# Performance work log

Measured on AMD Instinct MI355X. Metric: run time of the kernel, lower is better.

The kernel has to match this reference:

```python
import jax, jax.numpy as jnp
import numpy as np

NUM_HEADS = 16
HEAD_DIM = 64  # hidden_size 1024 / 16 heads


def setup_inputs() -> dict:
    key = jax.random.key(0)
    ks = jax.random.split(key, 5)
    B, S, D = 4, 2048, 1024
    std = 0.02
    return {
        "hidden_states": jax.random.normal(ks[0], (B, S, D), jnp.float32),
        "attention_mask": jnp.zeros((B, 1, 1, S), jnp.float32),
        "Wq": jax.random.normal(ks[1], (D, D), jnp.float32) * std,
        "bq": jnp.zeros((D,), jnp.float32),
        "Wk": jax.random.normal(ks[2], (D, D), jnp.float32) * std,
        "bk": jnp.zeros((D,), jnp.float32),
        "Wv": jax.random.normal(ks[3], (D, D), jnp.float32) * std,
        "bv": jnp.zeros((D,), jnp.float32),
    }


def _split_heads(x):
    # [B, S, H*dh] -> [B, H, S, dh]
    B, S, _ = x.shape
    return x.reshape(B, S, NUM_HEADS, HEAD_DIM).transpose(0, 2, 1, 3)


def reference(hidden_states, attention_mask, Wq, bq, Wk, bk, Wv, bv):
    q = _split_heads(hidden_states @ Wq + bq)  # [B,H,S,dh]
    k = _split_heads(hidden_states @ Wk + bk)
    v = _split_heads(hidden_states @ Wv + bv)
    scale = 1.0 / jnp.sqrt(jnp.asarray(HEAD_DIM, q.dtype))
    scores = jnp.einsum("bhqd,bhkd->bhqk", q, k) * scale
    scores = scores + attention_mask.astype(scores.dtype)
    probs = jax.nn.softmax(scores, axis=-1)  # dropout prob = 0 -> identity
    ctx = jnp.einsum("bhqk,bhkd->bhqd", probs, v)
    B, H, S, dh = ctx.shape
    return ctx.transpose(0, 2, 1, 3).reshape(B, S, H * dh)
```

## Files before the change

### kernel.cpp

```cpp
#include <hip/hip_runtime.h>
#include <stdint.h>

typedef unsigned short u16;
typedef __attribute__((ext_vector_type(4))) float f32x4;
typedef __attribute__((ext_vector_type(8))) short bf16x8;
typedef __attribute__((ext_vector_type(4))) short bf16x4;
typedef __attribute__((ext_vector_type(4))) int i32x4;

__device__ inline u16 f2b(float x) {
  union { float f; uint32_t u; } t; t.f = x;
  uint32_t r = t.u + 0x7FFFu + ((t.u >> 16) & 1u);
  return (u16)(r >> 16);
}

__global__ void cvt_hs_k(const float* __restrict__ in, u16* __restrict__ outp, int n) {
  int i = (blockIdx.x * 256 + threadIdx.x) * 4;
  if (i >= n) return;
  float4 v = *(const float4*)(in + i);
  ushort4 o = { f2b(v.x), f2b(v.y), f2b(v.z), f2b(v.w) };
  *(ushort4*)(outp + i) = o;
}

__global__ void twk(const float* __restrict__ Wq, const float* __restrict__ Wk,
                    const float* __restrict__ Wv, u16* __restrict__ Wt) {
  __shared__ float tile[64][65];
  const float* W = (blockIdx.z == 0) ? Wq : ((blockIdx.z == 1) ? Wk : Wv);
  int n0 = blockIdx.x * 64, k0 = blockIdx.y * 64;
  int tid = threadIdx.x;
#pragma unroll 4
  for (int i = 0; i < 16; ++i) {
    int idx = i * 256 + tid; int r = idx >> 6, c = idx & 63;
    tile[r][c] = W[(k0 + r) * 1024 + n0 + c];
  }
  __syncthreads();
  u16* dst = Wt + blockIdx.z * 1048576;
#pragma unroll 4
  for (int i = 0; i < 16; ++i) {
    int idx = i * 256 + tid; int r = idx >> 6, c = idx & 63;
    dst[(n0 + r) * 1024 + k0 + c] = f2b(tile[c][r]);
  }
}

__global__ __launch_bounds__(256) void qkv_gemm_k(
    const u16* __restrict__ hsb, const u16* __restrict__ wt,
    const float* __restrict__ bq, const float* __restrict__ bk, const float* __restrict__ bv,
    u16* __restrict__ Qo, u16* __restrict__ Ko, u16* __restrict__ Vto) {
  __shared__ u16 t1[128 * 64];
  __shared__ u16 t2[128 * 64];
  const int tid = threadIdx.x;
  const int w = tid >> 6, l = tid & 63, g = l >> 4, lm = l & 15;
  const int nbase = blockIdx.x * 128;
  const int wi = nbase >> 10;
  const int nloc0 = nbase & 1023;
  const int mbase = blockIdx.y * 128;
  const bool swapped = (wi < 2);
  const u16* T1g = swapped ? (wt + wi * 1048576 + nloc0 * 1024) : (hsb + mbase * 1024);
  const u16* T2g = swapped ? (hsb + mbase * 1024) : (wt + 2 * 1048576 + nloc0 * 1024);

  f32x4 acc[4][4];
#pragma unroll
  for (int i = 0; i < 4; ++i)
#pragma unroll
    for (int j = 0; j < 4; ++j)
#pragma unroll
      for (int r = 0; r < 4; ++r) acc[i][j][r] = 0.f;

  const int r1w = (w >> 1) * 64;
  const int r2w = (w & 1) * 64;

  for (int kb = 0; kb < 1024; kb += 64) {
    __syncthreads();
#pragma unroll
    for (int p = 0; p < 4; ++p) {
      int idx = p * 256 + tid;
      int r = idx >> 3, c = idx & 7;
      int sc = ((c ^ (r & 7)) * 8);
      *(i32x4*)(t1 + r * 64 + sc) = *(const i32x4*)(T1g + r * 1024 + kb + c * 8);
      *(i32x4*)(t2 + r * 64 + sc) = *(const i32x4*)(T2g + r * 1024 + kb + c * 8);
    }
    __syncthreads();
#pragma unroll
    for (int ks = 0; ks < 2; ++ks) {
      bf16x8 fa[4], fb[4];
#pragma unroll
      for (int i = 0; i < 4; ++i) {
        int ra = r1w + i * 16 + lm;
        fa[i] = *(const bf16x8*)(t1 + ra * 64 + (((g + 4 * ks) ^ (ra & 7)) * 8));
        int rb = r2w + i * 16 + lm;
        fb[i] = *(const bf16x8*)(t2 + rb * 64 + (((g + 4 * ks) ^ (rb & 7)) * 8));
      }
#pragma unroll
      for (int i = 0; i < 4; ++i)
#pragma unroll
        for (int j = 0; j < 4; ++j)
          acc[i][j] = __builtin_amdgcn_mfma_f32_16x16x32_bf16(fa[i], fb[j], acc[i][j], 0, 0, 0);
    }
  }

  if (swapped) {
    u16* O = (wi == 0) ? Qo : Ko;
    const float* bias = (wi == 0) ? bq : bk;
#pragma unroll
    for (int i = 0; i < 4; ++i) {
      int nl = nloc0 + r1w + i * 16 + g * 4;
      f32x4 bv4 = *(const f32x4*)(bias + nl);
      int d = nl & 63, h = nl >> 6;
#pragma unroll
      for (int j = 0; j < 4; ++j) {
        int m = mbase + r2w + j * 16 + lm;
        int bb = m >> 11, s = m & 2047;
        f32x4 v = acc[i][j];
        ushort4 o = { f2b(v[0] + bv4[0]), f2b(v[1] + bv4[1]),
                      f2b(v[2] + bv4[2]), f2b(v[3] + bv4[3]) };
        *(ushort4*)(O + ((size_t)(bb * 16 + h) * 2048 + s) * 64 + d) = o;
      }
    }
  } else {
#pragma unroll
    for (int j = 0; j < 4; ++j) {
      int nl = nloc0 + r2w + j * 16 + lm;
      float bias = bv[nl];
      int d = nl & 63, h = nl >> 6;
#pragma unroll
      for (int i = 0; i < 4; ++i) {
        int m = mbase + r1w + i * 16 + g * 4;
        int bb = m >> 11, s = m & 2047;
        f32x4 v = acc[i][j];
        ushort4 o = { f2b(v[0] + bias), f2b(v[1] + bias),
                      f2b(v[2] + bias), f2b(v[3] + bias) };
        *(ushort4*)(Vto + ((size_t)(bb * 16 + h) * 64 + d) * 2048 + s) = o;
      }
    }
  }
}

__global__ __launch_bounds__(256) void attn_k(
    const u16* __restrict__ Qg, const u16* __restrict__ Kg, const u16* __restrict__ Vtg,
    const float* __restrict__ maskg, float* __restrict__ outp) {
  __shared__ u16 kt[128 * 64];
  __shared__ u16 vt[64 * 128];
  __shared__ float mk[128];
  const int tid = threadIdx.x;
  const int w = tid >> 6, l = tid & 63, g = l >> 4, lm = l & 15;
  const int bh = blockIdx.y, b = bh >> 4, h = bh & 15;
  const int q0 = blockIdx.x * 64 + w * 16;
  const u16* Qb = Qg + ((size_t)bh * 2048 + q0) * 64;
  const u16* Kb = Kg + (size_t)bh * 2048 * 64;
  const u16* Vb = Vtg + (size_t)bh * 64 * 2048;
  const float* mb = maskg + b * 2048;

  bf16x8 qf0 = *(const bf16x8*)(Qb + lm * 64 + g * 8);
  bf16x8 qf1 = *(const bf16x8*)(Qb + lm * 64 + 32 + g * 8);

  f32x4 ctx[4];
#pragma unroll
  for (int dt = 0; dt < 4; ++dt)
#pragma unroll
    for (int r = 0; r < 4; ++r) ctx[dt][r] = 0.f;
  float mrun = -3.0e38f, lrun = 0.f;

  for (int kv = 0; kv < 2048; kv += 128) {
    __syncthreads();
#pragma unroll
    for (int p = 0; p < 4; ++p) {
      int idx = p * 256 + tid;
      { int r = idx >> 3, c = idx & 7;
        *(i32x4*)(kt + r * 64 + ((c ^ (r & 7)) * 8)) =
            *(const i32x4*)(Kb + (size_t)(kv + r) * 64 + c * 8); }
      { int r = idx >> 4, c = idx & 15;
        *(i32x4*)(vt + r * 128 + ((c ^ (r & 7)) * 8)) =
            *(const i32x4*)(Vb + (size_t)r * 2048 + kv + c * 8); }
    }
    if (tid < 128) mk[tid] = mb[kv + tid];
    __syncthreads();

    f32x4 st[8];
#pragma unroll
    for (int t = 0; t < 8; ++t)
#pragma unroll
      for (int r = 0; r < 4; ++r) st[t][r] = 0.f;

#pragma unroll
    for (int ks = 0; ks < 2; ++ks) {
      bf16x8 qf = ks ? qf1 : qf0;
#pragma unroll
      for (int t = 0; t < 8; ++t) {
        int r = t * 16 + lm;
        bf16x8 kf = *(const bf16x8*)(kt + r * 64 + (((g + 4 * ks) ^ (r & 7)) * 8));
        st[t] = __builtin_amdgcn_mfma_f32_16x16x32_bf16(kf, qf, st[t], 0, 0, 0);
      }
    }

    float tmax = -3.0e38f;
#pragma unroll
    for (int t = 0; t < 8; ++t) {
      f32x4 mv = *(const f32x4*)(mk + t * 16 + g * 4);
#pragma unroll
      for (int r = 0; r < 4; ++r) {
        float s = st[t][r] * 0.125f + mv[r];
        st[t][r] = s;
        tmax = fmaxf(tmax, s);
      }
    }
    tmax = fmaxf(tmax, __shfl_xor(tmax, 16));
    tmax = fmaxf(tmax, __shfl_xor(tmax, 32));
    float mnew = fmaxf(mrun, tmax);
    float corr = __expf(mrun - mnew);
    float lsum = 0.f;
    bf16x4 pt[8];
#pragma unroll
    for (int t = 0; t < 8; ++t)
#pragma unroll
      for (int r = 0; r < 4; ++r) {
        float p = __expf(st[t][r] - mnew);
        lsum += p;
        pt[t][r] = (short)f2b(p);
      }
    lsum += __shfl_xor(lsum, 16);
    lsum += __shfl_xor(lsum, 32);
    lrun = lrun * corr + lsum;
    mrun = mnew;
#pragma unroll
    for (int dt = 0; dt < 4; ++dt)
#pragma unroll
      for (int r = 0; r < 4; ++r) ctx[dt][r] *= corr;

#pragma unroll
    for (int tp = 0; tp < 4; ++tp) {
      int t0 = 2 * tp, t1 = 2 * tp + 1;
      bf16x8 pb;
#pragma unroll
      for (int i = 0; i < 4; ++i) { pb[i] = pt[t0][i]; pb[4 + i] = pt[t1][i]; }
#pragma unroll
      for (int dt = 0; dt < 4; ++dt) {
        int r = dt * 16 + lm;
        int base = r * 128;
        bf16x4 v0 = *(const bf16x4*)(vt + base + (((2 * t0 + (g >> 1)) ^ (r & 7)) * 8) + (g & 1) * 4);
        bf16x4 v1 = *(const bf16x4*)(vt + base + (((2 * t1 + (g >> 1)) ^ (r & 7)) * 8) + (g & 1) * 4);
        bf16x8 va;
#pragma unroll
        for (int i = 0; i < 4; ++i) { va[i] = v0[i]; va[4 + i] = v1[i]; }
        ctx[dt] = __builtin_amdgcn_mfma_f32_16x16x32_bf16(va, pb, ctx[dt], 0, 0, 0);
      }
    }
  }

  float inv = 1.f / lrun;
  int sq = q0 + lm;
  float* ob = outp + ((size_t)(b * 2048 + sq)) * 1024 + h * 64;
#pragma unroll
  for (int dt = 0; dt < 4; ++dt) {
    f32x4 o;
#pragma unroll
    for (int r = 0; r < 4; ++r) o[r] = ctx[dt][r] * inv;
    *(f32x4*)(ob + dt * 16 + g * 4) = o;
  }
}

extern "C" void kernel_launch(void* const* d_in, const int* in_sizes, int n_in,
                              void* d_out, int out_size, void* d_ws, size_t ws_size,
                              hipStream_t stream) {
  const float* hs   = (const float*)d_in[0];
  const float* mask = (const float*)d_in[1];
  const float* Wq   = (const float*)d_in[2];
  const float* bq   = (const float*)d_in[3];
  const float* Wk   = (const float*)d_in[4];
  const float* bk   = (const float*)d_in[5];
  const float* Wv   = (const float*)d_in[6];
  const float* bv   = (const float*)d_in[7];
  float* out = (float*)d_out;

  char* ws = (char*)d_ws;
  u16* hsb = (u16*)(ws);
  u16* wt  = (u16*)(ws + (16u << 20));
  u16* Qb  = (u16*)(ws + (24u << 20));
  u16* Kb  = (u16*)(ws + (40u << 20));
  u16* Vtb = (u16*)(ws + (56u << 20));

  cvt_hs_k<<<dim3(8192), dim3(256), 0, stream>>>(hs, hsb, 8388608);
  twk<<<dim3(16, 16, 3), dim3(256), 0, stream>>>(Wq, Wk, Wv, wt);
  qkv_gemm_k<<<dim3(24, 64), dim3(256), 0, stream>>>(hsb, wt, bq, bk, bv, Qb, Kb, Vtb);
  attn_k<<<dim3(32, 64), dim3(256), 0, stream>>>(Qb, Kb, Vtb, mask, out);
}
```

Measured before the change: 317.0 us.

## Use direct-to-LDS loads, exp2 softmax with lazy rescale, and permuted V layout

Global-to-shared copies in both the GEMM and the attention kernel now use global_load_lds with pre-swizzled source addresses, avoiding the register round trip. Attention works in the base-2 domain, using hardware v_exp_f32 and packed bf16 conversion, and skips the running-max rescale unless the max grows by more than 8. V^T is stored in a permuted column order so each PV operand becomes a single 16-byte LDS read. The kernels also gain block-index remapping for L2 locality, s_setprio around MFMA bursts, and 512-thread attention blocks covering 128 queries. The lazy rescale keeps unnormalized probabilities up to 2^8, which trades a small precision margin for fewer multiplies.

New measurement: 267.6 us. 15.6% less time.

```diff
diff --git a/kernel.cpp b/kernel.cpp
--- a/kernel.cpp
+++ b/kernel.cpp
@@ -4,13 +4,32 @@
 typedef unsigned short u16;
 typedef __attribute__((ext_vector_type(4))) float f32x4;
 typedef __attribute__((ext_vector_type(8))) short bf16x8;
-typedef __attribute__((ext_vector_type(4))) short bf16x4;
 typedef __attribute__((ext_vector_type(4))) int i32x4;
+
+#define LOG2E 1.4426950408889634f
 
 __device__ inline u16 f2b(float x) {
   union { float f; uint32_t u; } t; t.f = x;
   uint32_t r = t.u + 0x7FFFu + ((t.u >> 16) & 1u);
   return (u16)(r >> 16);
+}
+
+__device__ inline int cvtpk(float a, float b) {
+  int r;
+  asm("v_cvt_pk_bf16_f32 %0, %1, %2" : "=v"(r) : "v"(a), "v"(b));
+  return r;
+}
+
+__device__ inline float exp2a(float x) {
+  float r;
+  asm("v_exp_f32 %0, %1" : "=v"(r) : "v"(x));
+  return r;
+}
+
+typedef const __attribute__((address_space(1))) void* gas_t;
+typedef __attribute__((address_space(3))) void* las_t;
+__device__ inline void gld16(const void* g, void* l) {
+  __builtin_amdgcn_global_load_lds((gas_t)g, (las_t)l, 16, 0, 0);
 }
 
 __global__ void cvt_hs_k(const float* __restrict__ in, u16* __restrict__ outp, int n) {
@@ -49,10 +68,15 @@
   __shared__ u16 t2[128 * 64];
   const int tid = threadIdx.x;
   const int w = tid >> 6, l = tid & 63, g = l >> 4, lm = l & 15;
-  const int nbase = blockIdx.x * 128;
+
+  int lin = blockIdx.y * 24 + blockIdx.x;
+  lin = (lin & 7) * 192 + (lin >> 3);
+  const int bx = lin % 24, by = lin / 24;
+
+  const int nbase = bx * 128;
   const int wi = nbase >> 10;
   const int nloc0 = nbase & 1023;
-  const int mbase = blockIdx.y * 128;
+  const int mbase = by * 128;
   const bool swapped = (wi < 2);
   const u16* T1g = swapped ? (wt + wi * 1048576 + nloc0 * 1024) : (hsb + mbase * 1024);
   const u16* T2g = swapped ? (hsb + mbase * 1024) : (wt + 2 * 1048576 + nloc0 * 1024);
@@ -74,9 +98,9 @@
     for (int p = 0; p < 4; ++p) {
       int idx = p * 256 + tid;
       int r = idx >> 3, c = idx & 7;
-      int sc = ((c ^ (r & 7)) * 8);
-      *(i32x4*)(t1 + r * 64 + sc) = *(const i32x4*)(T1g + r * 1024 + kb + c * 8);
-      *(i32x4*)(t2 + r * 64 + sc) = *(const i32x4*)(T2g + r * 1024 + kb + c * 8);
+      int sc = (c ^ (r & 7)) << 3;
+      gld16(T1g + r * 1024 + kb + sc, t1 + idx * 8);
+      gld16(T2g + r * 1024 + kb + sc, t2 + idx * 8);
     }
     __syncthreads();
 #pragma unroll
@@ -85,15 +109,17 @@
 #pragma unroll
       for (int i = 0; i < 4; ++i) {
         int ra = r1w + i * 16 + lm;
-        fa[i] = *(const bf16x8*)(t1 + ra * 64 + (((g + 4 * ks) ^ (ra & 7)) * 8));
+        fa[i] = *(const bf16x8*)(t1 + ra * 64 + (((g + 4 * ks) ^ (ra & 7)) << 3));
         int rb = r2w + i * 16 + lm;
-        fb[i] = *(const bf16x8*)(t2 + rb * 64 + (((g + 4 * ks) ^ (rb & 7)) * 8));
-      }
+        fb[i] = *(const bf16x8*)(t2 + rb * 64 + (((g + 4 * ks) ^ (rb & 7)) << 3));
+      }
+      __builtin_amdgcn_s_setprio(1);
 #pragma unroll
       for (int i = 0; i < 4; ++i)
 #pragma unroll
         for (int j = 0; j < 4; ++j)
           acc[i][j] = __builtin_amdgcn_mfma_f32_16x16x32_bf16(fa[i], fb[j], acc[i][j], 0, 0, 0);
+      __builtin_amdgcn_s_setprio(0);
     }
   }
 
@@ -125,16 +151,17 @@
       for (int i = 0; i < 4; ++i) {
         int m = mbase + r1w + i * 16 + g * 4;
         int bb = m >> 11, s = m & 2047;
+        int cp = (s & ~31) | (((s >> 2) & 3) << 3) | (((s >> 4) & 1) << 2);
         f32x4 v = acc[i][j];
         ushort4 o = { f2b(v[0] + bias), f2b(v[1] + bias),
                       f2b(v[2] + bias), f2b(v[3] + bias) };
-        *(ushort4*)(Vto + ((size_t)(bb * 16 + h) * 64 + d) * 2048 + s) = o;
-      }
-    }
-  }
-}
-
-__global__ __launch_bounds__(256) void attn_k(
+        *(ushort4*)(Vto + ((size_t)(bb * 16 + h) * 64 + d) * 2048 + cp) = o;
+      }
+    }
+  }
+}
+
+__global__ __launch_bounds__(512) void attn_k(
     const u16* __restrict__ Qg, const u16* __restrict__ Kg, const u16* __restrict__ Vtg,
     const float* __restrict__ maskg, float* __restrict__ outp) {
   __shared__ u16 kt[128 * 64];
@@ -142,8 +169,12 @@
   __shared__ float mk[128];
   const int tid = threadIdx.x;
   const int w = tid >> 6, l = tid & 63, g = l >> 4, lm = l & 15;
-  const int bh = blockIdx.y, b = bh >> 4, h = bh & 15;
-  const int q0 = blockIdx.x * 64 + w * 16;
+
+  int bid = blockIdx.y * 16 + blockIdx.x;
+  bid = (bid & 7) * 128 + (bid >> 3);
+  const int bx = bid & 15, bh = bid >> 4;
+  const int b = bh >> 4, h = bh & 15;
+  const int q0 = bx * 128 + w * 16;
   const u16* Qb = Qg + ((size_t)bh * 2048 + q0) * 64;
   const u16* Kb = Kg + (size_t)bh * 2048 * 64;
   const u16* Vb = Vtg + (size_t)bh * 64 * 2048;
@@ -158,20 +189,19 @@
 #pragma unroll
     for (int r = 0; r < 4; ++r) ctx[dt][r] = 0.f;
   float mrun = -3.0e38f, lrun = 0.f;
+  const float QS = 0.125f * LOG2E;
 
   for (int kv = 0; kv < 2048; kv += 128) {
     __syncthreads();
 #pragma unroll
-    for (int p = 0; p < 4; ++p) {
-      int idx = p * 256 + tid;
-      { int r = idx >> 3, c = idx & 7;
-        *(i32x4*)(kt + r * 64 + ((c ^ (r & 7)) * 8)) =
-            *(const i32x4*)(Kb + (size_t)(kv + r) * 64 + c * 8); }
-      { int r = idx >> 4, c = idx & 15;
-        *(i32x4*)(vt + r * 128 + ((c ^ (r & 7)) * 8)) =
-            *(const i32x4*)(Vb + (size_t)r * 2048 + kv + c * 8); }
-    }
-    if (tid < 128) mk[tid] = mb[kv + tid];
+    for (int p = 0; p < 2; ++p) {
+      int idx = p * 512 + tid;
+      int rk = idx >> 3, ck = idx & 7;
+      gld16(Kb + (size_t)(kv + rk) * 64 + ((ck ^ (rk & 7)) << 3), kt + idx * 8);
+      int rv = idx >> 4, cv = idx & 15;
+      gld16(Vb + (size_t)rv * 2048 + kv + ((cv ^ (rv & 7)) << 3), vt + idx * 8);
+    }
+    if (tid < 128) mk[tid] = mb[kv + tid] * LOG2E;
     __syncthreads();
 
     f32x4 st[8];
@@ -180,69 +210,70 @@
 #pragma unroll
       for (int r = 0; r < 4; ++r) st[t][r] = 0.f;
 
+    __builtin_amdgcn_s_setprio(1);
 #pragma unroll
     for (int ks = 0; ks < 2; ++ks) {
       bf16x8 qf = ks ? qf1 : qf0;
 #pragma unroll
       for (int t = 0; t < 8; ++t) {
         int r = t * 16 + lm;
-        bf16x8 kf = *(const bf16x8*)(kt + r * 64 + (((g + 4 * ks) ^ (r & 7)) * 8));
+        bf16x8 kf = *(const bf16x8*)(kt + r * 64 + (((g + 4 * ks) ^ (r & 7)) << 3));
         st[t] = __builtin_amdgcn_mfma_f32_16x16x32_bf16(kf, qf, st[t], 0, 0, 0);
       }
     }
+    __builtin_amdgcn_s_setprio(0);
 
     float tmax = -3.0e38f;
 #pragma unroll
     for (int t = 0; t < 8; ++t) {
       f32x4 mv = *(const f32x4*)(mk + t * 16 + g * 4);
 #pragma unroll
-      for (int r = 0; r < 4; ++r) {
-        float s = st[t][r] * 0.125f + mv[r];
-        st[t][r] = s;
-        tmax = fmaxf(tmax, s);
-      }
+      for (int r = 0; r < 4; ++r) st[t][r] = fmaf(st[t][r], QS, mv[r]);
+      tmax = fmaxf(tmax, fmaxf(fmaxf(st[t][0], st[t][1]), fmaxf(st[t][2], st[t][3])));
     }
     tmax = fmaxf(tmax, __shfl_xor(tmax, 16));
     tmax = fmaxf(tmax, __shfl_xor(tmax, 32));
-    float mnew = fmaxf(mrun, tmax);
-    float corr = __expf(mrun - mnew);
+
+    if (!__all(tmax <= mrun + 8.0f)) {
+      float mnew = fmaxf(mrun, tmax);
+      float corr = exp2a(mrun - mnew);
+      lrun *= corr;
+#pragma unroll
+      for (int dt = 0; dt < 4; ++dt)
+#pragma unroll
+        for (int r = 0; r < 4; ++r) ctx[dt][r] *= corr;
+      mrun = mnew;
+    }
+
+    int pt[8][2];
     float lsum = 0.f;
-    bf16x4 pt[8];
-#pragma unroll
-    for (int t = 0; t < 8; ++t)
-#pragma unroll
-      for (int r = 0; r < 4; ++r) {
-        float p = __expf(st[t][r] - mnew);
-        lsum += p;
-        pt[t][r] = (short)f2b(p);
-      }
+#pragma unroll
+    for (int t = 0; t < 8; ++t) {
+      float p0 = exp2a(st[t][0] - mrun);
+      float p1 = exp2a(st[t][1] - mrun);
+      float p2 = exp2a(st[t][2] - mrun);
+      float p3 = exp2a(st[t][3] - mrun);
+      lsum += (p0 + p1) + (p2 + p3);
+      pt[t][0] = cvtpk(p0, p1);
+      pt[t][1] = cvtpk(p2, p3);
+    }
     lsum += __shfl_xor(lsum, 16);
     lsum += __shfl_xor(lsum, 32);
-    lrun = lrun * corr + lsum;
-    mrun = mnew;
-#pragma unroll
-    for (int dt = 0; dt < 4; ++dt)
-#pragma unroll
-      for (int r = 0; r < 4; ++r) ctx[dt][r] *= corr;
-
+    lrun += lsum;
+
+    __builtin_amdgcn_s_setprio(1);
 #pragma unroll
     for (int tp = 0; tp < 4; ++tp) {
-      int t0 = 2 * tp, t1 = 2 * tp + 1;
-      bf16x8 pb;
-#pragma unroll
-      for (int i = 0; i < 4; ++i) { pb[i] = pt[t0][i]; pb[4 + i] = pt[t1][i]; }
+      i32x4 pbi = { pt[2 * tp][0], pt[2 * tp][1], pt[2 * tp + 1][0], pt[2 * tp + 1][1] };
+      bf16x8 pb = __builtin_bit_cast(bf16x8, pbi);
 #pragma unroll
       for (int dt = 0; dt < 4; ++dt) {
         int r = dt * 16 + lm;
-        int base = r * 128;
-        bf16x4 v0 = *(const bf16x4*)(vt + base + (((2 * t0 + (g >> 1)) ^ (r & 7)) * 8) + (g & 1) * 4);
-        bf16x4 v1 = *(const bf16x4*)(vt + base + (((2 * t1 + (g >> 1)) ^ (r & 7)) * 8) + (g & 1) * 4);
-        bf16x8 va;
-#pragma unroll
-        for (int i = 0; i < 4; ++i) { va[i] = v0[i]; va[4 + i] = v1[i]; }
+        bf16x8 va = *(const bf16x8*)(vt + r * 128 + (((tp * 4 + g) ^ (r & 7)) << 3));
         ctx[dt] = __builtin_amdgcn_mfma_f32_16x16x32_bf16(va, pb, ctx[dt], 0, 0, 0);
       }
     }
+    __builtin_amdgcn_s_setprio(0);
   }
 
   float inv = 1.f / lrun;
@@ -280,5 +311,5 @@
   cvt_hs_k<<<dim3(8192), dim3(256), 0, stream>>>(hs, hsb, 8388608);
   twk<<<dim3(16, 16, 3), dim3(256), 0, stream>>>(Wq, Wk, Wv, wt);
   qkv_gemm_k<<<dim3(24, 64), dim3(256), 0, stream>>>(hsb, wt, bq, bk, bv, Qb, Kb, Vtb);
-  attn_k<<<dim3(32, 64), dim3(256), 0, stream>>>(Qb, Kb, Vtb, mask, out);
-}
+  attn_k<<<dim3(16, 64), dim3(512), 0, stream>>>(Qb, Kb, Vtb, mask, out);
+}
```
